# Optimization experiments

Measured on AMD Instinct MI355X. Metric: run time of the kernel, lower is better.

## Reference

```python
import jax, jax.numpy as jnp
import numpy as np

B, N, M, F, BF = 16, 1024, 12, 64, 128
N_CONV = 3
VOCAB = 100
BN_EPS = 1e-3  # keras BatchNormalization default epsilon


def _bn(x, gamma, beta):
    # inference-mode BN with moving_mean=0, moving_var=1 (keras defaults)
    return gamma * (x * (1.0 / jnp.sqrt(1.0 + BN_EPS))) + beta


def setup_inputs() -> dict:
    key = jax.random.key(0)
    ks = jax.random.split(key, 16)
    in_fea = 2 * F + BF
    inp = {
        'atom_types': jax.random.randint(ks[0], (B, N), 0, VOCAB, dtype=jnp.int32),
        'bond_fea': jax.random.normal(ks[1], (B, N, M, BF), dtype=jnp.float32),
        'nbr_list': jax.random.randint(ks[2], (B, N, M), 0, N, dtype=jnp.int32),
        'target_index': jax.random.randint(ks[3], (B, 64), 0, N, dtype=jnp.int32),
        'emb': jax.random.normal(ks[4], (VOCAB, F), dtype=jnp.float32) * 0.05,
        'core_w': jax.random.normal(ks[5], (N_CONV, in_fea, F), dtype=jnp.float32) / np.sqrt(in_fea),
        'core_b': jnp.zeros((N_CONV, F), dtype=jnp.float32),
        'filt_w': jax.random.normal(ks[6], (N_CONV, in_fea, 1), dtype=jnp.float32) / np.sqrt(in_fea),
        'filt_b': jnp.zeros((N_CONV, 1), dtype=jnp.float32),
        'bna_g': jnp.ones((N_CONV, F), dtype=jnp.float32),
        'bna_b': jnp.zeros((N_CONV, F), dtype=jnp.float32),
        'bnb_g': jnp.ones((N_CONV, F), dtype=jnp.float32),
        'bnb_b': jnp.zeros((N_CONV, F), dtype=jnp.float32),
        'dense_w': jax.random.normal(ks[7], (F, F), dtype=jnp.float32) / np.sqrt(F),
        'dense_b': jnp.zeros((F,), dtype=jnp.float32),
    }
    return inp


def _cgcnn_layer(x, bond_fea, nbr_list, cw, cb, fw, fb, bag, bab, bbg, bbb):
    # x: (B,N,F); bond_fea: (B,N,M,BF); nbr_list: (B,N,M)
    bidx = jnp.arange(x.shape[0])[:, None, None]
    atom_nbr = x[bidx, nbr_list]                       # (B,N,M,F) gather_nd
    atom_self = jnp.broadcast_to(x[:, :, None, :], atom_nbr.shape)
    total = jnp.concatenate([atom_self, atom_nbr, bond_fea], axis=-1)  # (B,N,M,2F+BF)
    core = total @ cw + cb                             # (B,N,M,F)
    filt = total @ fw + fb                             # (B,N,M,1)
    core = _bn(core, bag, bab)
    filt = jax.nn.softmax(filt, axis=2)                # softmax over neighbors
    core = jax.nn.relu(core)
    summed = jnp.mean(filt * core, axis=2)             # (B,N,F)
    summed = _bn(summed, bbg, bbb)
    return jax.nn.relu(x + summed)


def reference(atom_types, bond_fea, nbr_list, target_index, emb, core_w, core_b,
              filt_w, filt_b, bna_g, bna_b, bnb_g, bnb_b, dense_w, dense_b):
    x = emb[atom_types]                                # (B,N,F)
    for l in range(N_CONV):
        x = _cgcnn_layer(x, bond_fea, nbr_list, core_w[l], core_b[l],
                         filt_w[l], filt_b[l], bna_g[l], bna_b[l], bnb_g[l], bnb_b[l])
    bidx = jnp.arange(x.shape[0])[:, None]
    crys = x[bidx, target_index]                       # (B,N0,F) pooling gather
    crys = jax.nn.relu(crys)
    out = jax.nn.relu(crys @ dense_w + dense_b)        # (B,N0,F)
    return out
```

## Files before the change

### kernel.cpp

```cpp
#include <hip/hip_runtime.h>
#include <hip/hip_bf16.h>


#define BB 16
#define NN 1024
#define MM 12
#define FF 64
#define BFE 128
#define RT (BB * NN * MM)
#define S_BN 0.99950037f
#define WCOLS 208
#define WSTR 136

typedef __attribute__((ext_vector_type(8))) short bf16x8;
typedef __attribute__((ext_vector_type(4))) float f32x4;

static __device__ __forceinline__ unsigned short f2bf(float f) {
    union { float f; unsigned u; } c; c.f = f;
    unsigned r = c.u + 0x7fff + ((c.u >> 16) & 1);
    return (unsigned short)(r >> 16);
}
static __device__ __forceinline__ float bf2f(unsigned short s) {
    union { unsigned u; float f; } c; c.u = ((unsigned)s) << 16;
    return c.f;
}
static __device__ __forceinline__ bf16x8 pack_bf16x8(float4 a, float4 b) {
    union { unsigned u[4]; bf16x8 v; } r;
    r.u[0] = (unsigned)f2bf(a.x) | ((unsigned)f2bf(a.y) << 16);
    r.u[1] = (unsigned)f2bf(a.z) | ((unsigned)f2bf(a.w) << 16);
    r.u[2] = (unsigned)f2bf(b.x) | ((unsigned)f2bf(b.y) << 16);
    r.u[3] = (unsigned)f2bf(b.z) | ((unsigned)f2bf(b.w) << 16);
    return r.v;
}

__global__ void fold_w(const float* __restrict__ cw, const float* __restrict__ cb,
                       const float* __restrict__ g,  const float* __restrict__ bab,
                       float* __restrict__ cwp, float* __restrict__ cbp) {
    int i = blockIdx.x * 256 + threadIdx.x;
    if (i >= 3 * 256 * 64) return;
    int f = i & 63;
    int l = i / (256 * 64);
    float gs = g[l * 64 + f] * S_BN;
    cwp[i] = cw[i] * gs;
    if (((i >> 6) & 255) == 0)
        cbp[l * 64 + f] = cb[l * 64 + f] * gs + bab[l * 64 + f];
}

__global__ void prep_wT(const float* __restrict__ cw, const float* __restrict__ g,
                        const float* __restrict__ fw, unsigned short* __restrict__ wT) {
    int i = blockIdx.x * 256 + threadIdx.x;
    if (i >= WCOLS * WSTR) return;
    int col = i / WSTR, k = i % WSTR;
    float v = 0.f;
    if (k < 128) {
        if (col < 192) {
            int l = col >> 6, p = col & 63;
            int f = ((p & 15) << 2) | (p >> 4);
            v = cw[(l * 256 + 128 + k) * 64 + f] * g[l * 64 + f] * S_BN;
        } else if (col < 195) {
            int l = col - 192;
            v = fw[l * 256 + 128 + k];
        }
    }
    wT[i] = f2bf(v);
}

__global__ void embed_k(const int* __restrict__ at, const float* __restrict__ emb,
                        float* __restrict__ x) {
    int i = blockIdx.x * 256 + threadIdx.x;
    int f = i & 63;
    int bn = i >> 6;
    x[i] = emb[at[bn] * FF + f];
}

static __device__ __forceinline__ void store_tile(
    const f32x4* acc, unsigned short* __restrict__ core,
    float* __restrict__ filt, int crow, int m) {
    #pragma unroll
    for (int l = 0; l < 3; l++) {
        #pragma unroll
        for (int r = 0; r < 4; r++) {
            ushort4 h;
            h.x = f2bf(acc[l * 4 + 0][r]);
            h.y = f2bf(acc[l * 4 + 1][r]);
            h.z = f2bf(acc[l * 4 + 2][r]);
            h.w = f2bf(acc[l * 4 + 3][r]);
            *(ushort4*)&core[((size_t)l * RT + crow + r) * 64 + 4 * m] = h;
        }
    }
    if (m < 3) {
        #pragma unroll
        for (int r = 0; r < 4; r++)
            filt[(size_t)m * RT + crow + r] = acc[12][r];
    }
}

__global__ __launch_bounds__(256, 2) void gemm_bond(
    const float* __restrict__ bond, const unsigned short* __restrict__ wT,
    unsigned short* __restrict__ core, float* __restrict__ filt) {
    __shared__ unsigned short bsh[WCOLS * WSTR];
    int tid = threadIdx.x;
    int w = tid >> 6, lane = tid & 63;
    int m = lane & 15, quad = lane >> 4;

    const float4* wsrc = (const float4*)wT;
    float4* wdst = (float4*)bsh;
    #pragma unroll
    for (int i = 0; i < 14; i++) {
        int idx = tid + 256 * i;
        if (idx < (WCOLS * WSTR * 2) / 16) wdst[idx] = wsrc[idx];
    }
    __syncthreads();

    #pragma unroll 1
    for (int it = 0; it < 3; it++) {
        int row0 = blockIdx.x * 384 + it * 128;
        const float* abase = bond + (size_t)(row0 + w * 32 + m) * BFE + quad * 8;

        float4 areg[16];
        #pragma unroll
        for (int fr = 0; fr < 2; fr++) {
            #pragma unroll
            for (int c = 0; c < 4; c++) {
                areg[fr * 8 + c * 2 + 0] = *(const float4*)(abase + fr * 16 * BFE + c * 32);
                areg[fr * 8 + c * 2 + 1] = *(const float4*)(abase + fr * 16 * BFE + c * 32 + 4);
            }
        }
        bf16x8 af[2][4];
        #pragma unroll
        for (int fr = 0; fr < 2; fr++)
            #pragma unroll
            for (int c = 0; c < 4; c++)
                af[fr][c] = pack_bf16x8(areg[fr * 8 + c * 2], areg[fr * 8 + c * 2 + 1]);

        f32x4 acc0[13], acc1[13];
        #pragma unroll
        for (int t = 0; t < 13; t++) {
            acc0[t] = (f32x4){0.f, 0.f, 0.f, 0.f};
            acc1[t] = (f32x4){0.f, 0.f, 0.f, 0.f};
        }

        #pragma unroll
        for (int c = 0; c < 4; c++) {
            bf16x8 a0 = af[0][c], a1 = af[1][c];
            #pragma unroll
            for (int t = 0; t < 13; t++) {
                bf16x8 bfv = *(const bf16x8*)&bsh[(t * 16 + m) * WSTR + c * 32 + quad * 8];
                acc0[t] = __builtin_amdgcn_mfma_f32_16x16x32_bf16(a0, bfv, acc0[t], 0, 0, 0);
                acc1[t] = __builtin_amdgcn_mfma_f32_16x16x32_bf16(a1, bfv, acc1[t], 0, 0, 0);
            }
        }

        int crow = row0 + w * 32 + quad * 4;
        store_tile(acc0, core, filt, crow, m);
        store_tile(acc1, core, filt, crow + 16, m);
    }
}

__global__ __launch_bounds__(256) void atomproj(
    const float* __restrict__ x, const float* __restrict__ cwp_l,
    const float* __restrict__ cbp_l, const float* __restrict__ fw_l,
    const float* __restrict__ fb_l,
    float* __restrict__ ys, float* __restrict__ yn,
    float* __restrict__ fs, float* __restrict__ fn) {
    __shared__ float wsh[128 * 64];
    __shared__ float xs[4][64];
    int tid = threadIdx.x, w = tid >> 6, lane = tid & 63;
    #pragma unroll
    for (int i = 0; i < 8; i++)
        ((float4*)wsh)[tid + 256 * i] = ((const float4*)cwp_l)[tid + 256 * i];
    float fw1 = fw_l[lane], fw2 = fw_l[64 + lane];
    float cb = cbp_l[lane], fbv = fb_l[0];
    __syncthreads();
    #pragma unroll 1
    for (int it = 0; it < 4; it++) {
        int row = (blockIdx.x * 4 + it) * 4 + w;
        float xl = x[(size_t)row * 64 + lane];
        xs[w][lane] = xl;
        float a1 = cb, a2 = 0.f;
        #pragma unroll 16
        for (int k = 0; k < 64; k++) {
            float xv = xs[w][k];
            a1 += xv * wsh[k * 64 + lane];
            a2 += xv * wsh[(64 + k) * 64 + lane];
        }
        ys[(size_t)row * 64 + lane] = a1;
        yn[(size_t)row * 64 + lane] = a2;
        float p1 = xl * fw1, p2 = xl * fw2;
        #pragma unroll
        for (int off = 32; off; off >>= 1) {
            p1 += __shfl_xor(p1, off, 64);
            p2 += __shfl_xor(p2, off, 64);
        }
        if (lane == 0) { fs[row] = p1 + fbv; fn[row] = p2; }
    }
}

__global__ __launch_bounds__(256) void layer_ep(
    const float* __restrict__ x, const unsigned short* __restrict__ core_l,
    const float* __restrict__ filt_l, const int* __restrict__ nbr,
    const float* __restrict__ ys, const float* __restrict__ yn,
    const float* __restrict__ fs, const float* __restrict__ fn,
    const float* __restrict__ bbg, const float* __restrict__ bbb,
    float* __restrict__ xout) {
    int tid = threadIdx.x, w = tid >> 6, lane = tid & 63;
    int row = blockIdx.x * 4 + w;
    int base = (row >> 10) * NN;
    size_t rb = (size_t)row * MM;

    int jv[MM]; float fltv[MM], corev[MM];
    #pragma unroll
    for (int mm = 0; mm < MM; mm++) jv[mm] = nbr[rb + mm];
    float fsv = fs[row], ysv = ys[(size_t)row * 64 + lane];
    #pragma unroll
    for (int mm = 0; mm < MM; mm++)
        fltv[mm] = filt_l[rb + mm] + fsv + fn[base + jv[mm]];
    #pragma unroll
    for (int mm = 0; mm < MM; mm++)
        corev[mm] = bf2f(core_l[(rb + mm) * 64 + lane]) + ysv
                  + yn[(size_t)(base + jv[mm]) * 64 + lane];
    float fmax = -1e30f;
    #pragma unroll
    for (int mm = 0; mm < MM; mm++) fmax = fmaxf(fmax, fltv[mm]);
    float fsum = 0.f;
    #pragma unroll
    for (int mm = 0; mm < MM; mm++) { fltv[mm] = __expf(fltv[mm] - fmax); fsum += fltv[mm]; }
    float inv = 1.f / (12.f * fsum);
    float summed = 0.f;
    #pragma unroll
    for (int mm = 0; mm < MM; mm++) summed += fltv[mm] * fmaxf(corev[mm], 0.f);
    summed *= inv;
    float o = x[(size_t)row * 64 + lane] + bbg[lane] * (summed * S_BN) + bbb[lane];
    xout[(size_t)row * 64 + lane] = fmaxf(o, 0.f);
}

__global__ __launch_bounds__(256) void final_k(
    const float* __restrict__ x, const int* __restrict__ tidx,
    const float* __restrict__ dw, const float* __restrict__ db,
    float* __restrict__ out) {
    __shared__ float xs[4][64];
    __shared__ float wsh[64 * 64];
    int tid = threadIdx.x;
    int w = tid >> 6, lane = tid & 63;
    const float4* src = (const float4*)dw;
    float4* dst = (float4*)wsh;
    #pragma unroll
    for (int i = 0; i < 4; i++) dst[tid + 256 * i] = src[tid + 256 * i];
    int row = blockIdx.x * 4 + w;
    int b = row >> 6;
    int t = tidx[row];
    float xv = x[((size_t)b * NN + t) * 64 + lane];
    xs[w][lane] = fmaxf(xv, 0.f);
    __syncthreads();
    float a = db[lane];
    #pragma unroll 16
    for (int k = 0; k < 64; k++) a += xs[w][k] * wsh[k * 64 + lane];
    out[row * 64 + lane] = fmaxf(a, 0.f);
}

extern "C" void kernel_launch(void* const* d_in, const int* in_sizes, int n_in,
                              void* d_out, int out_size, void* d_ws, size_t ws_size,
                              hipStream_t stream) {
    const int*   at   = (const int*)d_in[0];
    const float* bond = (const float*)d_in[1];
    const int*   nbr  = (const int*)d_in[2];
    const int*   tgt  = (const int*)d_in[3];
    const float* emb  = (const float*)d_in[4];
    const float* cw   = (const float*)d_in[5];
    const float* cb   = (const float*)d_in[6];
    const float* fw   = (const float*)d_in[7];
    const float* fb   = (const float*)d_in[8];
    const float* bag  = (const float*)d_in[9];
    const float* bab  = (const float*)d_in[10];
    const float* bbg  = (const float*)d_in[11];
    const float* bbb  = (const float*)d_in[12];
    const float* dw   = (const float*)d_in[13];
    const float* db   = (const float*)d_in[14];

    float* ws   = (float*)d_ws;
    float* xA   = ws;
    float* xB   = xA + (size_t)BB * NN * FF;
    float* cwp  = xB + (size_t)BB * NN * FF;
    float* cbp  = cwp + 3 * 256 * 64;
    float* ys   = cbp + 192;
    float* yn   = ys + (size_t)BB * NN * FF;
    float* fs   = yn + (size_t)BB * NN * FF;
    float* fn   = fs + (size_t)BB * NN;
    float* filt = fn + (size_t)BB * NN;
    unsigned short* wT   = (unsigned short*)(filt + 3 * (size_t)RT);
    unsigned short* core = wT + WCOLS * WSTR;

    fold_w<<<(3 * 256 * 64 + 255) / 256, 256, 0, stream>>>(cw, cb, bag, bab, cwp, cbp);
    prep_wT<<<(WCOLS * WSTR + 255) / 256, 256, 0, stream>>>(cw, bag, fw, wT);
    embed_k<<<(BB * NN * FF) / 256, 256, 0, stream>>>(at, emb, xA);
    gemm_bond<<<512, 256, 0, stream>>>(bond, wT, core, filt);

    float* xin = xA;
    float* xout = xB;
    for (int l = 0; l < 3; l++) {
        atomproj<<<BB * NN / 16, 256, 0, stream>>>(
            xin, cwp + (size_t)l * 256 * 64, cbp + l * 64, fw + l * 256, fb + l,
            ys, yn, fs, fn);
        layer_ep<<<BB * NN / 4, 256, 0, stream>>>(
            xin, core + (size_t)l * RT * 64, filt + (size_t)l * RT, nbr,
            ys, yn, fs, fn, bbg + l * 64, bbb + l * 64, xout);
        float* t = xin; xin = xout; xout = t;
    }

    final_k<<<BB * 64 / 4, 256, 0, stream>>>(xin, tgt, dw, db, (float*)d_out);
}
```

Measured before the change: 348.1 us.

## Move atom projection onto MFMA with split-bf16 precision and shrink bond GEMM tile

Replaces the scalar FP32 atom-projection kernel with an MFMA bf16 kernel. It keeps near-FP32 accuracy by splitting x and the weights into hi/lo bf16 parts and issuing three MFMAs per tile. The weights are pre-packed once into a transposed, padded bf16 layout, and fold_w now only computes biases. The bond GEMM also processes 64-row steps with a single accumulator set instead of two, which lowers register pressure at the cost of more iterations.

```diff
diff --git a/kernel.cpp b/kernel.cpp
--- a/kernel.cpp
+++ b/kernel.cpp
@@ -11,6 +11,9 @@
 #define S_BN 0.99950037f
 #define WCOLS 208
 #define WSTR 136
+#define PCOLS 144
+#define PSTR 72
+#define PSZ (PCOLS * PSTR)
 
 typedef __attribute__((ext_vector_type(8))) short bf16x8;
 typedef __attribute__((ext_vector_type(4))) float f32x4;
@@ -32,18 +35,23 @@
     r.u[3] = (unsigned)f2bf(b.z) | ((unsigned)f2bf(b.w) << 16);
     return r.v;
 }
+static __device__ __forceinline__ float4 residual4(float4 v) {
+    float4 r;
+    r.x = v.x - bf2f(f2bf(v.x));
+    r.y = v.y - bf2f(f2bf(v.y));
+    r.z = v.z - bf2f(f2bf(v.z));
+    r.w = v.w - bf2f(f2bf(v.w));
+    return r;
+}
 
 __global__ void fold_w(const float* __restrict__ cw, const float* __restrict__ cb,
                        const float* __restrict__ g,  const float* __restrict__ bab,
-                       float* __restrict__ cwp, float* __restrict__ cbp) {
+                       float* __restrict__ cbp) {
     int i = blockIdx.x * 256 + threadIdx.x;
-    if (i >= 3 * 256 * 64) return;
-    int f = i & 63;
-    int l = i / (256 * 64);
+    if (i >= 3 * 64) return;
+    int f = i & 63, l = i >> 6;
     float gs = g[l * 64 + f] * S_BN;
-    cwp[i] = cw[i] * gs;
-    if (((i >> 6) & 255) == 0)
-        cbp[l * 64 + f] = cb[l * 64 + f] * gs + bab[l * 64 + f];
+    cbp[i] = cb[l * 64 + f] * gs + bab[l * 64 + f];
 }
 
 __global__ void prep_wT(const float* __restrict__ cw, const float* __restrict__ g,
@@ -65,34 +73,35 @@
     wT[i] = f2bf(v);
 }
 
+__global__ void prep_wproj(const float* __restrict__ cw, const float* __restrict__ g,
+                           const float* __restrict__ fw, unsigned short* __restrict__ wproj) {
+    int i = blockIdx.x * 256 + threadIdx.x;
+    if (i >= 3 * PSZ) return;
+    int l = i / PSZ;
+    int rem = i % PSZ;
+    int col = rem / PSTR, k = rem % PSTR;
+    float v = 0.f;
+    if (k < 64) {
+        if (col < 64)
+            v = cw[(l * 256 + k) * 64 + col] * g[l * 64 + col] * S_BN;
+        else if (col < 128)
+            v = cw[(l * 256 + 64 + k) * 64 + (col - 64)] * g[l * 64 + (col - 64)] * S_BN;
+        else if (col == 128)
+            v = fw[l * 256 + k];
+        else if (col == 129)
+            v = fw[l * 256 + 64 + k];
+    }
+    unsigned short hi = f2bf(v);
+    wproj[(size_t)l * 2 * PSZ + col * PSTR + k] = hi;
+    wproj[(size_t)l * 2 * PSZ + PSZ + col * PSTR + k] = f2bf(v - bf2f(hi));
+}
+
 __global__ void embed_k(const int* __restrict__ at, const float* __restrict__ emb,
                         float* __restrict__ x) {
     int i = blockIdx.x * 256 + threadIdx.x;
     int f = i & 63;
     int bn = i >> 6;
     x[i] = emb[at[bn] * FF + f];
-}
-
-static __device__ __forceinline__ void store_tile(
-    const f32x4* acc, unsigned short* __restrict__ core,
-    float* __restrict__ filt, int crow, int m) {
-    #pragma unroll
-    for (int l = 0; l < 3; l++) {
-        #pragma unroll
-        for (int r = 0; r < 4; r++) {
-            ushort4 h;
-            h.x = f2bf(acc[l * 4 + 0][r]);
-            h.y = f2bf(acc[l * 4 + 1][r]);
-            h.z = f2bf(acc[l * 4 + 2][r]);
-            h.w = f2bf(acc[l * 4 + 3][r]);
-            *(ushort4*)&core[((size_t)l * RT + crow + r) * 64 + 4 * m] = h;
-        }
-    }
-    if (m < 3) {
-        #pragma unroll
-        for (int r = 0; r < 4; r++)
-            filt[(size_t)m * RT + crow + r] = acc[12][r];
-    }
 }
 
 __global__ __launch_bounds__(256, 2) void gemm_bond(
@@ -113,86 +122,121 @@
     __syncthreads();
 
     #pragma unroll 1
-    for (int it = 0; it < 3; it++) {
-        int row0 = blockIdx.x * 384 + it * 128;
-        const float* abase = bond + (size_t)(row0 + w * 32 + m) * BFE + quad * 8;
-
-        float4 areg[16];
-        #pragma unroll
-        for (int fr = 0; fr < 2; fr++) {
-            #pragma unroll
-            for (int c = 0; c < 4; c++) {
-                areg[fr * 8 + c * 2 + 0] = *(const float4*)(abase + fr * 16 * BFE + c * 32);
-                areg[fr * 8 + c * 2 + 1] = *(const float4*)(abase + fr * 16 * BFE + c * 32 + 4);
-            }
-        }
-        bf16x8 af[2][4];
-        #pragma unroll
-        for (int fr = 0; fr < 2; fr++)
-            #pragma unroll
-            for (int c = 0; c < 4; c++)
-                af[fr][c] = pack_bf16x8(areg[fr * 8 + c * 2], areg[fr * 8 + c * 2 + 1]);
-
-        f32x4 acc0[13], acc1[13];
-        #pragma unroll
-        for (int t = 0; t < 13; t++) {
-            acc0[t] = (f32x4){0.f, 0.f, 0.f, 0.f};
-            acc1[t] = (f32x4){0.f, 0.f, 0.f, 0.f};
-        }
-
+    for (int it = 0; it < 6; it++) {
+        int row0 = blockIdx.x * 384 + it * 64;
+        const float* abase = bond + (size_t)(row0 + w * 16 + m) * BFE + quad * 8;
+
+        bf16x8 af[4];
         #pragma unroll
         for (int c = 0; c < 4; c++) {
-            bf16x8 a0 = af[0][c], a1 = af[1][c];
+            float4 v0 = *(const float4*)(abase + c * 32);
+            float4 v1 = *(const float4*)(abase + c * 32 + 4);
+            af[c] = pack_bf16x8(v0, v1);
+        }
+
+        f32x4 acc[13];
+        #pragma unroll
+        for (int t = 0; t < 13; t++) acc[t] = (f32x4){0.f, 0.f, 0.f, 0.f};
+
+        #pragma unroll
+        for (int c = 0; c < 4; c++) {
+            bf16x8 a = af[c];
             #pragma unroll
             for (int t = 0; t < 13; t++) {
                 bf16x8 bfv = *(const bf16x8*)&bsh[(t * 16 + m) * WSTR + c * 32 + quad * 8];
-                acc0[t] = __builtin_amdgcn_mfma_f32_16x16x32_bf16(a0, bfv, acc0[t], 0, 0, 0);
-                acc1[t] = __builtin_amdgcn_mfma_f32_16x16x32_bf16(a1, bfv, acc1[t], 0, 0, 0);
+                acc[t] = __builtin_amdgcn_mfma_f32_16x16x32_bf16(a, bfv, acc[t], 0, 0, 0);
             }
         }
 
-        int crow = row0 + w * 32 + quad * 4;
-        store_tile(acc0, core, filt, crow, m);
-        store_tile(acc1, core, filt, crow + 16, m);
-    }
-}
-
-__global__ __launch_bounds__(256) void atomproj(
-    const float* __restrict__ x, const float* __restrict__ cwp_l,
-    const float* __restrict__ cbp_l, const float* __restrict__ fw_l,
-    const float* __restrict__ fb_l,
+        int crow = row0 + w * 16 + quad * 4;
+        #pragma unroll
+        for (int l = 0; l < 3; l++) {
+            #pragma unroll
+            for (int r = 0; r < 4; r++) {
+                ushort4 h;
+                h.x = f2bf(acc[l * 4 + 0][r]);
+                h.y = f2bf(acc[l * 4 + 1][r]);
+                h.z = f2bf(acc[l * 4 + 2][r]);
+                h.w = f2bf(acc[l * 4 + 3][r]);
+                *(ushort4*)&core[((size_t)l * RT + crow + r) * 64 + 4 * m] = h;
+            }
+        }
+        if (m < 3) {
+            #pragma unroll
+            for (int r = 0; r < 4; r++)
+                filt[(size_t)m * RT + crow + r] = acc[12][r];
+        }
+    }
+}
+
+__global__ __launch_bounds__(256) void atomproj_mfma(
+    const float* __restrict__ x, const unsigned short* __restrict__ wproj_l,
+    const float* __restrict__ cbp_l, const float* __restrict__ fb_l,
     float* __restrict__ ys, float* __restrict__ yn,
     float* __restrict__ fs, float* __restrict__ fn) {
-    __shared__ float wsh[128 * 64];
-    __shared__ float xs[4][64];
+    __shared__ unsigned short psh[2 * PSZ];
     int tid = threadIdx.x, w = tid >> 6, lane = tid & 63;
-    #pragma unroll
-    for (int i = 0; i < 8; i++)
-        ((float4*)wsh)[tid + 256 * i] = ((const float4*)cwp_l)[tid + 256 * i];
-    float fw1 = fw_l[lane], fw2 = fw_l[64 + lane];
-    float cb = cbp_l[lane], fbv = fb_l[0];
+    int m = lane & 15, quad = lane >> 4;
+
+    const float4* src = (const float4*)wproj_l;
+    float4* dst = (float4*)psh;
+    #pragma unroll
+    for (int i = 0; i < 11; i++) {
+        int idx = tid + 256 * i;
+        if (idx < (2 * PSZ * 2) / 16) dst[idx] = src[idx];
+    }
     __syncthreads();
-    #pragma unroll 1
-    for (int it = 0; it < 4; it++) {
-        int row = (blockIdx.x * 4 + it) * 4 + w;
-        float xl = x[(size_t)row * 64 + lane];
-        xs[w][lane] = xl;
-        float a1 = cb, a2 = 0.f;
-        #pragma unroll 16
-        for (int k = 0; k < 64; k++) {
-            float xv = xs[w][k];
-            a1 += xv * wsh[k * 64 + lane];
-            a2 += xv * wsh[(64 + k) * 64 + lane];
-        }
-        ys[(size_t)row * 64 + lane] = a1;
-        yn[(size_t)row * 64 + lane] = a2;
-        float p1 = xl * fw1, p2 = xl * fw2;
-        #pragma unroll
-        for (int off = 32; off; off >>= 1) {
-            p1 += __shfl_xor(p1, off, 64);
-            p2 += __shfl_xor(p2, off, 64);
-        }
-        if (lane == 0) { fs[row] = p1 + fbv; fn[row] = p2; }
+
+    int row = blockIdx.x * 64 + w * 16 + m;
+    const float* xb = x + (size_t)row * 64 + quad * 8;
+    bf16x8 ahi[2], alo[2];
+    #pragma unroll
+    for (int c = 0; c < 2; c++) {
+        float4 v0 = *(const float4*)(xb + c * 32);
+        float4 v1 = *(const float4*)(xb + c * 32 + 4);
+        ahi[c] = pack_bf16x8(v0, v1);
+        alo[c] = pack_bf16x8(residual4(v0), residual4(v1));
+    }
+
+    f32x4 acc[9];
+    #pragma unroll
+    for (int t = 0; t < 9; t++) acc[t] = (f32x4){0.f, 0.f, 0.f, 0.f};
+
+    #pragma unroll
+    for (int c = 0; c < 2; c++) {
+        #pragma unroll
+        for (int t = 0; t < 9; t++) {
+            int off = (t * 16 + m) * PSTR + c * 32 + quad * 8;
+            bf16x8 bh = *(const bf16x8*)&psh[off];
+            bf16x8 bl = *(const bf16x8*)&psh[PSZ + off];
+            acc[t] = __builtin_amdgcn_mfma_f32_16x16x32_bf16(ahi[c], bh, acc[t], 0, 0, 0);
+            acc[t] = __builtin_amdgcn_mfma_f32_16x16x32_bf16(alo[c], bh, acc[t], 0, 0, 0);
+            acc[t] = __builtin_amdgcn_mfma_f32_16x16x32_bf16(ahi[c], bl, acc[t], 0, 0, 0);
+        }
+    }
+
+    int crow = blockIdx.x * 64 + w * 16 + quad * 4;
+    #pragma unroll
+    for (int t = 0; t < 4; t++) {
+        float bias = cbp_l[t * 16 + m];
+        #pragma unroll
+        for (int r = 0; r < 4; r++)
+            ys[(size_t)(crow + r) * 64 + t * 16 + m] = acc[t][r] + bias;
+    }
+    #pragma unroll
+    for (int t = 4; t < 8; t++) {
+        #pragma unroll
+        for (int r = 0; r < 4; r++)
+            yn[(size_t)(crow + r) * 64 + (t - 4) * 16 + m] = acc[t][r];
+    }
+    if (m == 0) {
+        float fbv = fb_l[0];
+        #pragma unroll
+        for (int r = 0; r < 4; r++) fs[crow + r] = acc[8][r] + fbv;
+    }
+    if (m == 1) {
+        #pragma unroll
+        for (int r = 0; r < 4; r++) fn[crow + r] = acc[8][r];
     }
 }
 
@@ -289,8 +333,10 @@
     float* filt = fn + (size_t)BB * NN;
     unsigned short* wT   = (unsigned short*)(filt + 3 * (size_t)RT);
     unsigned short* core = wT + WCOLS * WSTR;
-
-    fold_w<<<(3 * 256 * 64 + 255) / 256, 256, 0, stream>>>(cw, cb, bag, bab, cwp, cbp);
+    unsigned short* wproj = (unsigned short*)cwp;
+
+    fold_w<<<1, 256, 0, stream>>>(cw, cb, bag, bab, cbp);
+    prep_wproj<<<(3 * PSZ + 255) / 256, 256, 0, stream>>>(cw, bag, fw, wproj);
     prep_wT<<<(WCOLS * WSTR + 255) / 256, 256, 0, stream>>>(cw, bag, fw, wT);
     embed_k<<<(BB * NN * FF) / 256, 256, 0, stream>>>(at, emb, xA);
     gemm_bond<<<512, 256, 0, stream>>>(bond, wT, core, filt);
@@ -298,8 +344,8 @@
     float* xin = xA;
     float* xout = xB;
     for (int l = 0; l < 3; l++) {
-        atomproj<<<BB * NN / 16, 256, 0, stream>>>(
-            xin, cwp + (size_t)l * 256 * 64, cbp + l * 64, fw + l * 256, fb + l,
+        atomproj_mfma<<<BB * NN / 64, 256, 0, stream>>>(
+            xin, wproj + (size_t)l * 2 * PSZ, cbp + l * 64, fb + l,
             ys, yn, fs, fn);
         layer_ep<<<BB * NN / 4, 256, 0, stream>>>(
             xin, core + (size_t)l * RT * 64, filt + (size_t)l * RT, nbr,
```

New measurement: 279.9 us. 19.6% less time.
